# Optimization experiments

Measured on AMD Instinct MI355X. Metric: run time of the kernel, lower is better.

The kernel has to match this reference:

```python
import jax, jax.numpy as jnp
import numpy as np

N_SUBJECTS = 16
N_LABELS = 8
DENS_TEMP = 0.1  # args.ProtoSim_dens_temp


def setup_inputs() -> dict:
    key = jax.random.key(0)
    k1, k2, k3 = jax.random.split(key, 3)
    B, C, D = 16384, 2, 1024
    X_data = jax.random.normal(k1, (B, C, D), dtype=jnp.float32)
    subject = jax.random.randint(k2, (B,), 0, N_SUBJECTS, dtype=jnp.int64) if jax.config.jax_enable_x64 else jax.random.randint(k2, (B,), 0, N_SUBJECTS).astype(jnp.int32)
    labels = jax.random.randint(k3, (B,), 0, N_LABELS).astype(subject.dtype)
    return {"X_data": X_data, "subject": subject, "labels": labels}


def reference(X_data, subject, labels):
    B, C, D = X_data.shape
    K = N_SUBJECTS * N_LABELS  # all (subject,label) groups assumed present
    # contrast_feature = cat(unbind(X_data, 1), 0) -> [B*C, D]
    feat = X_data.swapaxes(0, 1).reshape(B * C, D)
    sub2 = jnp.tile(subject, C)          # cat((subject, subject))
    lab2 = jnp.tile(labels, C)
    # torch.unique sorts -> group g = subject * N_LABELS + label matches loop order
    gid = sub2 * N_LABELS + lab2
    counts = jax.ops.segment_sum(jnp.ones((B * C,), feat.dtype), gid, num_segments=K)  # (K,)
    centroid = jax.ops.segment_sum(feat, gid, num_segments=K) / counts[:, None]       # (K, D)
    # per-row euclidean distance to own group centroid (torch.cdist to 1 point)
    dist = jnp.linalg.norm(feat - centroid[gid], axis=1)                               # (B*C,)
    mean_sqrt = jax.ops.segment_sum(jnp.sqrt(dist), gid, num_segments=K) / counts
    density = mean_sqrt / jnp.log(counts + 10.0)
    density = jnp.where(counts <= 1.0, density.max(), density)
    density = jnp.clip(density, jnp.quantile(density, 0.1), jnp.quantile(density, 0.9))
    density = DENS_TEMP * density / density.mean()                                     # (K,)
    # masks: positives = same label, different subject
    g_sub = jnp.arange(K) // N_LABELS
    g_lab = jnp.arange(K) % N_LABELS
    subj_mask = (sub2[:, None] != g_sub[None, :]).astype(feat.dtype)  # (B*C, K)
    lab_mask = (lab2[:, None] == g_lab[None, :]).astype(feat.dtype)
    mask = subj_mask * lab_mask
    # every row has N_SUBJECTS-1 positives (all groups present), so no row filtering
    sim = (feat @ centroid.T) / density[None, :]                                        # (B*C, K)
    sim = sim - sim.max(axis=1, keepdims=True)
    pos = sim * mask
    logp = jax.nn.log_softmax(pos, axis=1)
    row_loss = -(mask * logp).sum(axis=1) / mask.sum(axis=1)  # soft-target CE / #pos
    return row_loss.reshape(C, B).mean()
```

## Files before the change

kernel.cpp:

```cpp
#include <hip/hip_runtime.h>
#include <hip/hip_bf16.h>
#include <math.h>

#define NSUB 16
#define NLAB 8
#define KG 128
#define BN 16384
#define DD 1024

typedef float v4f __attribute__((ext_vector_type(4)));
typedef short short8v __attribute__((ext_vector_type(8)));

static __device__ __forceinline__ short f2bf(float f) {
    unsigned u = __builtin_bit_cast(unsigned, f);
    unsigned r = (u + 0x7fffu + ((u >> 16) & 1u)) >> 16;
    return (short)r;
}

static __device__ __forceinline__ short8v pack_bf8(float4 lo, float4 hi) {
    union { short8v s; __hip_bfloat162 h[4]; } u;
    u.h[0] = __float22bfloat162_rn(float2{lo.x, lo.y});
    u.h[1] = __float22bfloat162_rn(float2{lo.z, lo.w});
    u.h[2] = __float22bfloat162_rn(float2{hi.x, hi.y});
    u.h[3] = __float22bfloat162_rn(float2{hi.z, hi.w});
    return u.s;
}

__global__ __launch_bounds__(1024) void k0_gid(const int* __restrict__ subject,
                                               const int* __restrict__ labels,
                                               int* __restrict__ gid, int* __restrict__ cnt) {
    __shared__ int h[KG];
    int t = threadIdx.x;
    if (t < KG) h[t] = 0;
    __syncthreads();
    int b = blockIdx.x * 1024 + t;
    int g = subject[b] * NLAB + labels[b];
    gid[b] = g;
    atomicAdd(&h[g], 1);
    __syncthreads();
    if (t < KG && h[t]) atomicAdd(&cnt[t], h[t]);
}

__global__ void k0b_offs(const int* __restrict__ cnt, int* __restrict__ offs,
                         int* __restrict__ cursor) {
    __shared__ int c[KG];
    int t = threadIdx.x;
    c[t] = cnt[t];
    __syncthreads();
    int o = 0;
    for (int j = 0; j < t; ++j) o += c[j];
    offs[t] = o;
    cursor[t] = o;
}

__global__ __launch_bounds__(1024) void k0c_scatter(const int* __restrict__ gid,
                                                    int* __restrict__ cursor,
                                                    int* __restrict__ rowlist) {
    __shared__ int lcnt[KG], lbase[KG], lcur[KG];
    int t = threadIdx.x;
    if (t < KG) { lcnt[t] = 0; lcur[t] = 0; }
    __syncthreads();
    int b = blockIdx.x * 1024 + t;
    int g = gid[b];
    atomicAdd(&lcnt[g], 1);
    __syncthreads();
    if (t < KG) lbase[t] = lcnt[t] ? atomicAdd(&cursor[t], lcnt[t]) : 0;
    __syncthreads();
    int pos = lbase[g] + atomicAdd(&lcur[g], 1);
    rowlist[pos] = b;
}

__global__ __launch_bounds__(256) void k1_centroid(const float* __restrict__ X,
                                                   const int* __restrict__ rowlist,
                                                   const int* __restrict__ offs,
                                                   const int* __restrict__ cnt,
                                                   float* __restrict__ centroid) {
    int g = blockIdx.x >> 2;
    int dq = blockIdx.x & 3;
    int d = dq * 256 + threadIdx.x;
    __shared__ int rows[512];
    int n = cnt[g], o = offs[g];
    if (n > 512) n = 512;
    for (int i = threadIdx.x; i < n; i += 256) rows[i] = rowlist[o + i];
    __syncthreads();
    float acc = 0.f;
    int i = 0;
    for (; i + 8 <= n; i += 8) {
        float v[16];
#pragma unroll
        for (int u = 0; u < 8; ++u) {
            size_t base = (size_t)rows[i + u] * 2048 + d;
            v[2 * u] = X[base];
            v[2 * u + 1] = X[base + 1024];
        }
#pragma unroll
        for (int u = 0; u < 16; ++u) acc += v[u];
    }
    for (; i < n; ++i) {
        size_t base = (size_t)rows[i] * 2048 + d;
        acc += X[base] + X[base + 1024];
    }
    centroid[(size_t)g * DD + d] = acc / (2.f * (float)n);
}

__global__ __launch_bounds__(256) void k2b_cbf(const float* __restrict__ centroid,
                                               unsigned short* __restrict__ Cbf) {
    int i = blockIdx.x * 256 + threadIdx.x;
    Cbf[i] = (unsigned short)f2bf(centroid[i]);
}

__global__ __launch_bounds__(256) void k3_dist(const float* __restrict__ X,
                                               const int* __restrict__ rowlist,
                                               const int* __restrict__ offs,
                                               const int* __restrict__ cnt,
                                               const float* __restrict__ centroid,
                                               float* __restrict__ sqrtsum) {
    int g = blockIdx.x >> 3;
    int ch = blockIdx.x & 7;
    int t = threadIdx.x, w = t >> 6, lane = t & 63;
    __shared__ float cent[DD];
    __shared__ int rows[512];
    __shared__ float bsum;
    for (int i = t; i < DD; i += 256) cent[i] = centroid[(size_t)g * DD + i];
    int n = cnt[g], o = offs[g];
    if (n > 512) n = 512;
    for (int i = t; i < n; i += 256) rows[i] = rowlist[o + i];
    if (t == 0) bsum = 0.f;
    __syncthreads();
    int nf = 2 * n, cw = ch * 4 + w;
    float wacc = 0.f;
    for (int fi = cw; fi < nf; fi += 32) {
        int b = rows[fi >> 1], c = fi & 1;
        const float* xp = X + (size_t)b * 2048 + (size_t)c * 1024;
        float acc = 0.f;
#pragma unroll
        for (int c4 = 0; c4 < 4; ++c4) {
            int d0 = c4 * 256 + lane * 4;
            float4 xv = *(const float4*)(xp + d0);
            float4 cv = *(const float4*)&cent[d0];
            float dx = xv.x - cv.x, dy = xv.y - cv.y, dz = xv.z - cv.z, dw = xv.w - cv.w;
            acc += dx * dx + dy * dy + dz * dz + dw * dw;
        }
#pragma unroll
        for (int m = 32; m; m >>= 1) acc += __shfl_xor(acc, m, 64);
        if (lane == 0) wacc += sqrtf(sqrtf(acc));
    }
    if (lane == 0 && wacc != 0.f) atomicAdd(&bsum, wacc);
    __syncthreads();
    if (t == 0) atomicAdd(&sqrtsum[g], bsum);
}

__global__ void k4_density(const float* __restrict__ sqrtsum,
                           const int* __restrict__ cnt,
                           float* __restrict__ recipDen) {
    __shared__ float tmp[KG];
    __shared__ float d1s[KG];
    __shared__ float qv[4];
    int g = threadIdx.x;
    float cntf = 2.f * (float)cnt[g];
    float d0 = (sqrtsum[g] / cntf) / logf(cntf + 10.f);
    tmp[g] = d0;
    __syncthreads();
    float dmax = -INFINITY;
    for (int j = 0; j < KG; ++j) dmax = fmaxf(dmax, tmp[j]);
    float v = (cntf <= 1.f) ? dmax : d0;
    d1s[g] = v;
    __syncthreads();
    int less = 0, eq = 0;
    for (int j = 0; j < KG; ++j) {
        float u = d1s[j];
        less += (u < v) ? 1 : 0;
        eq += (u == v) ? 1 : 0;
    }
    const int ppos[4] = {12, 13, 114, 115};
    for (int q = 0; q < 4; ++q)
        if (less <= ppos[q] && ppos[q] < less + eq) qv[q] = v;
    __syncthreads();
    float q10 = 0.3f * qv[0] + 0.7f * qv[1];
    float q90 = 0.7f * qv[2] + 0.3f * qv[3];
    float d2 = fminf(fmaxf(v, q10), q90);
    __syncthreads();
    tmp[g] = d2;
    __syncthreads();
    float sum = 0.f;
    for (int j = 0; j < KG; ++j) sum += tmp[j];
    float mean = sum / (float)KG;
    float den = 0.1f * d2 / mean;
    recipDen[g] = 1.f / den;
}

__global__ __launch_bounds__(256) void k5_loss(const float* __restrict__ X,
                                               const unsigned short* __restrict__ Cbf,
                                               const int* __restrict__ gid,
                                               const float* __restrict__ recipDen,
                                               float* __restrict__ out) {
    __shared__ float bs;
    if (threadIdx.x == 0) bs = 0.f;
    __syncthreads();
    int t = threadIdx.x, lane = t & 63;
    int gw = blockIdx.x * 4 + (t >> 6);
    int row0 = gw * 32;
    int m = lane & 15, q = lane >> 4;
    int r0 = row0 + m, r1 = row0 + 16 + m;
    const float* a0p = X + (size_t)(r0 & (BN - 1)) * 2048 + (size_t)(r0 >> 14) * 1024 + q * 8;
    const float* a1p = X + (size_t)(r1 & (BN - 1)) * 2048 + (size_t)(r1 >> 14) * 1024 + q * 8;
    const unsigned short* bp = Cbf + (size_t)m * DD + q * 8;

    v4f acc[2][8];
#pragma unroll
    for (int i = 0; i < 2; ++i)
#pragma unroll
        for (int j = 0; j < 8; ++j) acc[i][j] = (v4f){0.f, 0.f, 0.f, 0.f};

    float4 a0l = *(const float4*)(a0p), a0h = *(const float4*)(a0p + 4);
    float4 a1l = *(const float4*)(a1p), a1h = *(const float4*)(a1p + 4);
    short8v cb[8];
#pragma unroll
    for (int gt = 0; gt < 8; ++gt) cb[gt] = *(const short8v*)(bp + gt * 16 * DD);
    short8v ca0 = pack_bf8(a0l, a0h), ca1 = pack_bf8(a1l, a1h);

    for (int kc = 0; kc < 31; ++kc) {
        int k = (kc + 1) * 32;
        float4 na0l = *(const float4*)(a0p + k), na0h = *(const float4*)(a0p + k + 4);
        float4 na1l = *(const float4*)(a1p + k), na1h = *(const float4*)(a1p + k + 4);
        short8v nb[8];
#pragma unroll
        for (int gt = 0; gt < 8; ++gt) nb[gt] = *(const short8v*)(bp + gt * 16 * DD + k);
#pragma unroll
        for (int gt = 0; gt < 8; ++gt) {
            acc[0][gt] = __builtin_amdgcn_mfma_f32_16x16x32_bf16(ca0, cb[gt], acc[0][gt], 0, 0, 0);
            acc[1][gt] = __builtin_amdgcn_mfma_f32_16x16x32_bf16(ca1, cb[gt], acc[1][gt], 0, 0, 0);
        }
        ca0 = pack_bf8(na0l, na0h);
        ca1 = pack_bf8(na1l, na1h);
#pragma unroll
        for (int gt = 0; gt < 8; ++gt) cb[gt] = nb[gt];
    }
#pragma unroll
    for (int gt = 0; gt < 8; ++gt) {
        acc[0][gt] = __builtin_amdgcn_mfma_f32_16x16x32_bf16(ca0, cb[gt], acc[0][gt], 0, 0, 0);
        acc[1][gt] = __builtin_amdgcn_mfma_f32_16x16x32_bf16(ca1, cb[gt], acc[1][gt], 0, 0, 0);
    }

    float cden[8];
#pragma unroll
    for (int gt = 0; gt < 8; ++gt) cden[gt] = recipDen[gt * 16 + m];
    float ll = 0.f;
#pragma unroll
    for (int tile = 0; tile < 2; ++tile) {
#pragma unroll
        for (int reg = 0; reg < 4; ++reg) {
            int row = row0 + tile * 16 + q * 4 + reg;
            int b = row & (BN - 1);
            int gb = gid[b];
            int s = gb >> 3, l = gb & 7;
            float sim[8];
            float mx = -INFINITY;
#pragma unroll
            for (int gt = 0; gt < 8; ++gt) {
                sim[gt] = acc[tile][gt][reg] * cden[gt];
                mx = fmaxf(mx, sim[gt]);
            }
#pragma unroll
            for (int x = 1; x < 16; x <<= 1) mx = fmaxf(mx, __shfl_xor(mx, x, 64));
            float S = 0.f, P = 0.f;
#pragma unroll
            for (int gt = 0; gt < 8; ++gt) {
                int g = gt * 16 + m;
                if (((g & 7) == l) && ((g >> 3) != s)) {
                    float pv = sim[gt] - mx;
                    S += expf(pv);
                    P += pv;
                }
            }
#pragma unroll
            for (int x = 1; x < 16; x <<= 1) {
                S += __shfl_xor(S, x, 64);
                P += __shfl_xor(P, x, 64);
            }
            if (m == 0) ll += logf(113.f + S) - P * (1.f / 15.f);
        }
    }
    ll += __shfl_xor(ll, 16, 64);
    ll += __shfl_xor(ll, 32, 64);
    if (lane == 0) atomicAdd(&bs, ll);
    __syncthreads();
    if (t == 0) atomicAdd(out, bs * (1.f / 32768.f));
}

extern "C" void kernel_launch(void* const* d_in, const int* in_sizes, int n_in,
                              void* d_out, int out_size, void* d_ws, size_t ws_size,
                              hipStream_t stream) {
    const float* X = (const float*)d_in[0];
    const int* subject = (const int*)d_in[1];
    const int* labels = (const int*)d_in[2];
    float* out = (float*)d_out;
    char* w = (char*)d_ws;
    int* gid = (int*)(w + 0);
    int* cnt = (int*)(w + 65536);
    int* offs = (int*)(w + 66048);
    int* cursor = (int*)(w + 66560);
    float* sqrtsum = (float*)(w + 67072);
    float* recipDen = (float*)(w + 67584);
    int* rowlist = (int*)(w + 131072);
    float* centroid = (float*)(w + 262144);
    unsigned short* Cbf = (unsigned short*)(w + 786432);

    hipMemsetAsync(cnt, 0, KG * sizeof(int), stream);
    hipMemsetAsync(sqrtsum, 0, KG * sizeof(float), stream);
    hipMemsetAsync(out, 0, sizeof(float), stream);

    k0_gid<<<16, 1024, 0, stream>>>(subject, labels, gid, cnt);
    k0b_offs<<<1, KG, 0, stream>>>(cnt, offs, cursor);
    k0c_scatter<<<16, 1024, 0, stream>>>(gid, cursor, rowlist);
    k1_centroid<<<KG * 4, 256, 0, stream>>>(X, rowlist, offs, cnt, centroid);
    k2b_cbf<<<KG * DD / 256, 256, 0, stream>>>(centroid, Cbf);
    k3_dist<<<KG * 8, 256, 0, stream>>>(X, rowlist, offs, cnt, centroid, sqrtsum);
    k4_density<<<1, KG, 0, stream>>>(sqrtsum, cnt, recipDen);
    k5_loss<<<256, 256, 0, stream>>>(X, Cbf, gid, recipDen, out);
}
```

Measured before the change: 289.9 us.

## Compute distances from GEMM dot products and norms, removing second X pass

Replaces the separate per-group distance kernel, which re-read X, with the expansion |x-c|^2 = |x|^2 - 2x·c + |c|^2. The dot products come from a single bf16 MFMA GEMM that also accumulates fp32 row norms. The full row-by-128 Dot matrix is stored to workspace and reused by both the distance pass and a new loss kernel, so X is read once instead of twice. The cost is a 16 MB Dot write and read. Distances now rest on bf16-rounded dot products and can suffer cancellation, which the clamp to zero only partly guards.

```diff
diff --git a/kernel.cpp b/kernel.cpp
--- a/kernel.cpp
+++ b/kernel.cpp
@@ -24,6 +24,10 @@
     u.h[2] = __float22bfloat162_rn(float2{hi.x, hi.y});
     u.h[3] = __float22bfloat162_rn(float2{hi.z, hi.w});
     return u.s;
+}
+
+static __device__ __forceinline__ float dot4(float4 v) {
+    return v.x * v.x + v.y * v.y + v.z * v.z + v.w * v.w;
 }
 
 __global__ __launch_bounds__(1024) void k0_gid(const int* __restrict__ subject,
@@ -104,50 +108,109 @@
 }
 
 __global__ __launch_bounds__(256) void k2b_cbf(const float* __restrict__ centroid,
-                                               unsigned short* __restrict__ Cbf) {
-    int i = blockIdx.x * 256 + threadIdx.x;
-    Cbf[i] = (unsigned short)f2bf(centroid[i]);
-}
-
-__global__ __launch_bounds__(256) void k3_dist(const float* __restrict__ X,
-                                               const int* __restrict__ rowlist,
-                                               const int* __restrict__ offs,
-                                               const int* __restrict__ cnt,
-                                               const float* __restrict__ centroid,
-                                               float* __restrict__ sqrtsum) {
-    int g = blockIdx.x >> 3;
-    int ch = blockIdx.x & 7;
-    int t = threadIdx.x, w = t >> 6, lane = t & 63;
-    __shared__ float cent[DD];
-    __shared__ int rows[512];
-    __shared__ float bsum;
-    for (int i = t; i < DD; i += 256) cent[i] = centroid[(size_t)g * DD + i];
-    int n = cnt[g], o = offs[g];
-    if (n > 512) n = 512;
-    for (int i = t; i < n; i += 256) rows[i] = rowlist[o + i];
-    if (t == 0) bsum = 0.f;
-    __syncthreads();
-    int nf = 2 * n, cw = ch * 4 + w;
-    float wacc = 0.f;
-    for (int fi = cw; fi < nf; fi += 32) {
-        int b = rows[fi >> 1], c = fi & 1;
-        const float* xp = X + (size_t)b * 2048 + (size_t)c * 1024;
-        float acc = 0.f;
-#pragma unroll
-        for (int c4 = 0; c4 < 4; ++c4) {
-            int d0 = c4 * 256 + lane * 4;
-            float4 xv = *(const float4*)(xp + d0);
-            float4 cv = *(const float4*)&cent[d0];
-            float dx = xv.x - cv.x, dy = xv.y - cv.y, dz = xv.z - cv.z, dw = xv.w - cv.w;
-            acc += dx * dx + dy * dy + dz * dz + dw * dw;
+                                               unsigned short* __restrict__ Cbf,
+                                               float* __restrict__ cnorm) {
+    __shared__ float wsum[4];
+    int g = blockIdx.x, t = threadIdx.x;
+    float4 v = *(const float4*)(centroid + (size_t)g * DD + t * 4);
+    short4 bv = make_short4(f2bf(v.x), f2bf(v.y), f2bf(v.z), f2bf(v.w));
+    *(short4*)(Cbf + (size_t)g * DD + t * 4) = bv;
+    float s = dot4(v);
+#pragma unroll
+    for (int x = 32; x; x >>= 1) s += __shfl_xor(s, x, 64);
+    int lane = t & 63, w = t >> 6;
+    if (lane == 0) wsum[w] = s;
+    __syncthreads();
+    if (t == 0) cnorm[g] = wsum[0] + wsum[1] + wsum[2] + wsum[3];
+}
+
+__global__ __launch_bounds__(256) void k5a_dot(const float* __restrict__ X,
+                                               const unsigned short* __restrict__ Cbf,
+                                               float* __restrict__ Dot,
+                                               float* __restrict__ rownorm) {
+    int t = threadIdx.x, lane = t & 63;
+    int gw = blockIdx.x * 4 + (t >> 6);
+    int row0 = gw * 32;
+    int m = lane & 15, q = lane >> 4;
+    int r0 = row0 + m, r1 = row0 + 16 + m;
+    const float* a0p = X + (size_t)(r0 & (BN - 1)) * 2048 + (size_t)(r0 >> 14) * 1024 + q * 8;
+    const float* a1p = X + (size_t)(r1 & (BN - 1)) * 2048 + (size_t)(r1 >> 14) * 1024 + q * 8;
+    const unsigned short* bp = Cbf + (size_t)m * DD + q * 8;
+
+    v4f acc[2][8];
+#pragma unroll
+    for (int i = 0; i < 2; ++i)
+#pragma unroll
+        for (int j = 0; j < 8; ++j) acc[i][j] = (v4f){0.f, 0.f, 0.f, 0.f};
+
+    float s0 = 0.f, s1 = 0.f;
+    float4 a0l = *(const float4*)(a0p), a0h = *(const float4*)(a0p + 4);
+    float4 a1l = *(const float4*)(a1p), a1h = *(const float4*)(a1p + 4);
+    s0 += dot4(a0l) + dot4(a0h);
+    s1 += dot4(a1l) + dot4(a1h);
+    short8v cb[8];
+#pragma unroll
+    for (int gt = 0; gt < 8; ++gt) cb[gt] = *(const short8v*)(bp + gt * 16 * DD);
+    short8v ca0 = pack_bf8(a0l, a0h), ca1 = pack_bf8(a1l, a1h);
+
+    for (int kc = 0; kc < 31; ++kc) {
+        int k = (kc + 1) * 32;
+        float4 na0l = *(const float4*)(a0p + k), na0h = *(const float4*)(a0p + k + 4);
+        float4 na1l = *(const float4*)(a1p + k), na1h = *(const float4*)(a1p + k + 4);
+        short8v nb[8];
+#pragma unroll
+        for (int gt = 0; gt < 8; ++gt) nb[gt] = *(const short8v*)(bp + gt * 16 * DD + k);
+#pragma unroll
+        for (int gt = 0; gt < 8; ++gt) {
+            acc[0][gt] = __builtin_amdgcn_mfma_f32_16x16x32_bf16(ca0, cb[gt], acc[0][gt], 0, 0, 0);
+            acc[1][gt] = __builtin_amdgcn_mfma_f32_16x16x32_bf16(ca1, cb[gt], acc[1][gt], 0, 0, 0);
         }
-#pragma unroll
-        for (int m = 32; m; m >>= 1) acc += __shfl_xor(acc, m, 64);
-        if (lane == 0) wacc += sqrtf(sqrtf(acc));
-    }
-    if (lane == 0 && wacc != 0.f) atomicAdd(&bsum, wacc);
-    __syncthreads();
-    if (t == 0) atomicAdd(&sqrtsum[g], bsum);
+        s0 += dot4(na0l) + dot4(na0h);
+        s1 += dot4(na1l) + dot4(na1h);
+        ca0 = pack_bf8(na0l, na0h);
+        ca1 = pack_bf8(na1l, na1h);
+#pragma unroll
+        for (int gt = 0; gt < 8; ++gt) cb[gt] = nb[gt];
+    }
+#pragma unroll
+    for (int gt = 0; gt < 8; ++gt) {
+        acc[0][gt] = __builtin_amdgcn_mfma_f32_16x16x32_bf16(ca0, cb[gt], acc[0][gt], 0, 0, 0);
+        acc[1][gt] = __builtin_amdgcn_mfma_f32_16x16x32_bf16(ca1, cb[gt], acc[1][gt], 0, 0, 0);
+    }
+
+    s0 += __shfl_xor(s0, 16, 64); s0 += __shfl_xor(s0, 32, 64);
+    s1 += __shfl_xor(s1, 16, 64); s1 += __shfl_xor(s1, 32, 64);
+    if (lane < 16) rownorm[r0] = s0;
+    else if (lane < 32) rownorm[r1] = s1;
+
+#pragma unroll
+    for (int tile = 0; tile < 2; ++tile)
+#pragma unroll
+        for (int reg = 0; reg < 4; ++reg) {
+            int row = row0 + tile * 16 + q * 4 + reg;
+#pragma unroll
+            for (int gt = 0; gt < 8; ++gt)
+                Dot[(size_t)row * KG + gt * 16 + m] = acc[tile][gt][reg];
+        }
+}
+
+__global__ __launch_bounds__(1024) void k3b_dist(const float* __restrict__ Dot,
+                                                 const float* __restrict__ rownorm,
+                                                 const float* __restrict__ cnorm,
+                                                 const int* __restrict__ gid,
+                                                 float* __restrict__ sqrtsum) {
+    __shared__ float h[KG];
+    int t = threadIdx.x;
+    if (t < KG) h[t] = 0.f;
+    __syncthreads();
+    int r = blockIdx.x * 1024 + t;
+    int b = r & (BN - 1);
+    int g = gid[b];
+    float d2 = rownorm[r] - 2.f * Dot[(size_t)r * KG + g] + cnorm[g];
+    d2 = fmaxf(d2, 0.f);
+    atomicAdd(&h[g], sqrtf(sqrtf(d2)));
+    __syncthreads();
+    if (t < KG && h[t] != 0.f) atomicAdd(&sqrtsum[t], h[t]);
 }
 
 __global__ void k4_density(const float* __restrict__ sqrtsum,
@@ -189,103 +252,39 @@
     recipDen[g] = 1.f / den;
 }
 
-__global__ __launch_bounds__(256) void k5_loss(const float* __restrict__ X,
-                                               const unsigned short* __restrict__ Cbf,
-                                               const int* __restrict__ gid,
-                                               const float* __restrict__ recipDen,
-                                               float* __restrict__ out) {
-    __shared__ float bs;
-    if (threadIdx.x == 0) bs = 0.f;
-    __syncthreads();
-    int t = threadIdx.x, lane = t & 63;
-    int gw = blockIdx.x * 4 + (t >> 6);
-    int row0 = gw * 32;
-    int m = lane & 15, q = lane >> 4;
-    int r0 = row0 + m, r1 = row0 + 16 + m;
-    const float* a0p = X + (size_t)(r0 & (BN - 1)) * 2048 + (size_t)(r0 >> 14) * 1024 + q * 8;
-    const float* a1p = X + (size_t)(r1 & (BN - 1)) * 2048 + (size_t)(r1 >> 14) * 1024 + q * 8;
-    const unsigned short* bp = Cbf + (size_t)m * DD + q * 8;
-
-    v4f acc[2][8];
-#pragma unroll
-    for (int i = 0; i < 2; ++i)
-#pragma unroll
-        for (int j = 0; j < 8; ++j) acc[i][j] = (v4f){0.f, 0.f, 0.f, 0.f};
-
-    float4 a0l = *(const float4*)(a0p), a0h = *(const float4*)(a0p + 4);
-    float4 a1l = *(const float4*)(a1p), a1h = *(const float4*)(a1p + 4);
-    short8v cb[8];
-#pragma unroll
-    for (int gt = 0; gt < 8; ++gt) cb[gt] = *(const short8v*)(bp + gt * 16 * DD);
-    short8v ca0 = pack_bf8(a0l, a0h), ca1 = pack_bf8(a1l, a1h);
-
-    for (int kc = 0; kc < 31; ++kc) {
-        int k = (kc + 1) * 32;
-        float4 na0l = *(const float4*)(a0p + k), na0h = *(const float4*)(a0p + k + 4);
-        float4 na1l = *(const float4*)(a1p + k), na1h = *(const float4*)(a1p + k + 4);
-        short8v nb[8];
-#pragma unroll
-        for (int gt = 0; gt < 8; ++gt) nb[gt] = *(const short8v*)(bp + gt * 16 * DD + k);
-#pragma unroll
-        for (int gt = 0; gt < 8; ++gt) {
-            acc[0][gt] = __builtin_amdgcn_mfma_f32_16x16x32_bf16(ca0, cb[gt], acc[0][gt], 0, 0, 0);
-            acc[1][gt] = __builtin_amdgcn_mfma_f32_16x16x32_bf16(ca1, cb[gt], acc[1][gt], 0, 0, 0);
-        }
-        ca0 = pack_bf8(na0l, na0h);
-        ca1 = pack_bf8(na1l, na1h);
-#pragma unroll
-        for (int gt = 0; gt < 8; ++gt) cb[gt] = nb[gt];
-    }
-#pragma unroll
-    for (int gt = 0; gt < 8; ++gt) {
-        acc[0][gt] = __builtin_amdgcn_mfma_f32_16x16x32_bf16(ca0, cb[gt], acc[0][gt], 0, 0, 0);
-        acc[1][gt] = __builtin_amdgcn_mfma_f32_16x16x32_bf16(ca1, cb[gt], acc[1][gt], 0, 0, 0);
-    }
-
-    float cden[8];
-#pragma unroll
-    for (int gt = 0; gt < 8; ++gt) cden[gt] = recipDen[gt * 16 + m];
+__global__ __launch_bounds__(256) void k5b_loss(const float* __restrict__ Dot,
+                                                const int* __restrict__ gid,
+                                                const float* __restrict__ recipDen,
+                                                float* __restrict__ out) {
+    __shared__ float wsum[4];
+    int t = threadIdx.x, lane = t & 63, w = t >> 6;
+    int gwave = blockIdx.x * 4 + w;
+    int g0 = lane, g1 = 64 + lane;
+    float rd0 = recipDen[g0], rd1 = recipDen[g1];
+    int s0g = g0 >> 3, l0g = g0 & 7, s1g = g1 >> 3, l1g = g1 & 7;
     float ll = 0.f;
-#pragma unroll
-    for (int tile = 0; tile < 2; ++tile) {
-#pragma unroll
-        for (int reg = 0; reg < 4; ++reg) {
-            int row = row0 + tile * 16 + q * 4 + reg;
-            int b = row & (BN - 1);
-            int gb = gid[b];
-            int s = gb >> 3, l = gb & 7;
-            float sim[8];
-            float mx = -INFINITY;
-#pragma unroll
-            for (int gt = 0; gt < 8; ++gt) {
-                sim[gt] = acc[tile][gt][reg] * cden[gt];
-                mx = fmaxf(mx, sim[gt]);
-            }
-#pragma unroll
-            for (int x = 1; x < 16; x <<= 1) mx = fmaxf(mx, __shfl_xor(mx, x, 64));
-            float S = 0.f, P = 0.f;
-#pragma unroll
-            for (int gt = 0; gt < 8; ++gt) {
-                int g = gt * 16 + m;
-                if (((g & 7) == l) && ((g >> 3) != s)) {
-                    float pv = sim[gt] - mx;
-                    S += expf(pv);
-                    P += pv;
-                }
-            }
-#pragma unroll
-            for (int x = 1; x < 16; x <<= 1) {
-                S += __shfl_xor(S, x, 64);
-                P += __shfl_xor(P, x, 64);
-            }
-            if (m == 0) ll += logf(113.f + S) - P * (1.f / 15.f);
-        }
-    }
-    ll += __shfl_xor(ll, 16, 64);
-    ll += __shfl_xor(ll, 32, 64);
-    if (lane == 0) atomicAdd(&bs, ll);
-    __syncthreads();
-    if (t == 0) atomicAdd(out, bs * (1.f / 32768.f));
+    for (int i = 0; i < 32; ++i) {
+        int row = gwave * 32 + i;
+        int b = row & (BN - 1);
+        int gb = gid[b];
+        int s = gb >> 3, l = gb & 7;
+        float sim0 = Dot[(size_t)row * KG + g0] * rd0;
+        float sim1 = Dot[(size_t)row * KG + g1] * rd1;
+        float mx = fmaxf(sim0, sim1);
+#pragma unroll
+        for (int x = 1; x < 64; x <<= 1) mx = fmaxf(mx, __shfl_xor(mx, x, 64));
+        bool p0 = (l0g == l) && (s0g != s);
+        bool p1 = (l1g == l) && (s1g != s);
+        float S = 0.f, P = 0.f;
+        if (p0) { float pv = sim0 - mx; S += expf(pv); P += pv; }
+        if (p1) { float pv = sim1 - mx; S += expf(pv); P += pv; }
+#pragma unroll
+        for (int x = 1; x < 64; x <<= 1) { S += __shfl_xor(S, x, 64); P += __shfl_xor(P, x, 64); }
+        if (lane == 0) ll += logf(113.f + S) - P * (1.f / 15.f);
+    }
+    if (lane == 0) wsum[w] = ll;
+    __syncthreads();
+    if (t == 0) atomicAdd(out, (wsum[0] + wsum[1] + wsum[2] + wsum[3]) * (1.f / 32768.f));
 }
 
 extern "C" void kernel_launch(void* const* d_in, const int* in_sizes, int n_in,
@@ -302,9 +301,12 @@
     int* cursor = (int*)(w + 66560);
     float* sqrtsum = (float*)(w + 67072);
     float* recipDen = (float*)(w + 67584);
+    float* cnorm = (float*)(w + 68096);
     int* rowlist = (int*)(w + 131072);
     float* centroid = (float*)(w + 262144);
     unsigned short* Cbf = (unsigned short*)(w + 786432);
+    float* rownorm = (float*)(w + 1048576);
+    float* Dot = (float*)(w + 2097152);
 
     hipMemsetAsync(cnt, 0, KG * sizeof(int), stream);
     hipMemsetAsync(sqrtsum, 0, KG * sizeof(float), stream);
@@ -314,8 +316,9 @@
     k0b_offs<<<1, KG, 0, stream>>>(cnt, offs, cursor);
     k0c_scatter<<<16, 1024, 0, stream>>>(gid, cursor, rowlist);
     k1_centroid<<<KG * 4, 256, 0, stream>>>(X, rowlist, offs, cnt, centroid);
-    k2b_cbf<<<KG * DD / 256, 256, 0, stream>>>(centroid, Cbf);
-    k3_dist<<<KG * 8, 256, 0, stream>>>(X, rowlist, offs, cnt, centroid, sqrtsum);
+    k2b_cbf<<<KG, 256, 0, stream>>>(centroid, Cbf, cnorm);
+    k5a_dot<<<256, 256, 0, stream>>>(X, Cbf, Dot, rownorm);
+    k3b_dist<<<32, 1024, 0, stream>>>(Dot, rownorm, cnorm, gid, sqrtsum);
     k4_density<<<1, KG, 0, stream>>>(sqrtsum, cnt, recipDen);
-    k5_loss<<<256, 256, 0, stream>>>(X, Cbf, gid, recipDen, out);
-}
+    k5b_loss<<<256, 256, 0, stream>>>(Dot, gid, recipDen, out);
+}
```

After: 290.2 us. About the same (+0.1%).
